# Kernel optimization log

Hardware: AMD Instinct MI355X
Metric: run time of the kernel (lower is better)

Reference implementation:

```python
import jax, jax.numpy as jnp
import numpy as np

D_MODEL = 1024
N_HEADS = 16
HEAD_DIM = D_MODEL // N_HEADS  # 64
ROT = HEAD_DIM // 2            # RotaryEmbedding(dim=head_dim//2) -> rot_dim = 32
THETA = 10000.0
BS, CTX, CACHE_LEN = 8, 1, 4096


def _rope(x, offset):
    """lucidrains rotate_queries_or_keys: rotate first ROT dims of head_dim,
    interleaved pair convention (x0,x1)->(-x1,x0), freqs repeated pairwise."""
    s = x.shape[2]
    inv_freq = 1.0 / (THETA ** (jnp.arange(0, ROT, 2, dtype=jnp.float32) / ROT))  # [ROT//2]
    t = offset + jnp.arange(s, dtype=jnp.float32)
    freqs = jnp.repeat(t[:, None] * inv_freq[None, :], 2, axis=-1)  # [s, ROT]
    cos, sin = jnp.cos(freqs), jnp.sin(freqs)
    x1, x2 = x[..., :ROT], x[..., ROT:]
    xr = x1.reshape(*x1.shape[:-1], ROT // 2, 2)
    rh = jnp.stack([-xr[..., 1], xr[..., 0]], axis=-1).reshape(x1.shape)
    return jnp.concatenate([x1 * cos + rh * sin, x2], axis=-1)


def setup_inputs() -> dict:
    key = jax.random.key(0)
    ks = jax.random.split(key, 11)
    w = lambda k, shp: jax.random.normal(k, shp, dtype=jnp.float32) * 0.02
    return {
        "q": jax.random.normal(ks[0], (BS, CTX, D_MODEL), dtype=jnp.float32),
        "k_cache": jax.random.normal(ks[1], (BS, N_HEADS, CACHE_LEN, HEAD_DIM), dtype=jnp.float32),
        "v_cache": jax.random.normal(ks[2], (BS, N_HEADS, CACHE_LEN, HEAD_DIM), dtype=jnp.float32),
        "WQ_w": w(ks[3], (D_MODEL, D_MODEL)), "WQ_b": w(ks[4], (D_MODEL,)),
        "WK_w": w(ks[5], (D_MODEL, D_MODEL)), "WK_b": w(ks[6], (D_MODEL,)),
        "WV_w": w(ks[7], (D_MODEL, D_MODEL)), "WV_b": w(ks[8], (D_MODEL,)),
        "WO_w": w(ks[9], (D_MODEL, D_MODEL)), "WO_b": w(ks[10], (D_MODEL,)),
    }


def reference(q, k_cache, v_cache, WQ_w, WQ_b, WK_w, WK_b, WV_w, WV_b, WO_w, WO_b):
    bs, context, dim = q.shape
    # last=True path: only the final token queries; k/v computed from the full input
    q_in = q[:, -1:, :]
    offset = (context - 1) + k_cache.shape[2]
    to_heads = lambda x: x.reshape(bs, -1, N_HEADS, HEAD_DIM).transpose(0, 2, 1, 3)
    qh = to_heads(q_in @ WQ_w.T + WQ_b)             # [b,h,1,hd]
    kh = to_heads(q @ WK_w.T + WK_b)                # [b,h,ctx,hd]
    vh = to_heads(q @ WV_w.T + WV_b)
    k = jnp.concatenate([k_cache, kh], axis=2)      # [b,h,S,hd]
    v = jnp.concatenate([v_cache, vh], axis=2)
    q_rot = _rope(qh, offset)
    k_rot = _rope(k, 0)                             # RoPE re-applied to full cache
    scale = 1.0 / np.sqrt(HEAD_DIM)
    scores = jnp.einsum('bhqd,bhkd->bhqk', q_rot, k_rot) * scale
    attn = jax.nn.softmax(scores, axis=-1)          # is_causal=False (decode step)
    out = jnp.einsum('bhqk,bhkd->bhqd', attn, v)
    out = out.transpose(0, 2, 1, 3).reshape(bs, -1, dim)
    return out @ WO_w.T + WO_b
```

## Files before the change

kernel.cpp:

```cpp
#include <hip/hip_runtime.h>
#include <hip/hip_bf16.h>
#include <math.h>

#define NH    16
#define HD    64
#define DM    1024
#define BSZ   8
#define CL    4096
#define SPLIT 8
#define CHUNK (CL / SPLIT)
#define PSTRIDE 68

#define WS_QH   0
#define WS_KH   8192
#define WS_VH   16384
#define WS_QROT 24576
#define WS_KROT 32768
#define WS_PART 40960
#define WS_HEAD (40960 + 128 * SPLIT * PSTRIDE)
#define WS_FLAG (WS_HEAD + 8192)

#define LOG2_THETA 13.287712379549449
#define TWO_PI     6.283185307179586476925286766559
#define SM_SCALE_L2 (0.125f * 1.4426950408889634f)

__device__ __forceinline__ void bf2x(unsigned u, float& a, float& b) {
  union { unsigned i; float f; } lo, hi;
  lo.i = u << 16;
  hi.i = u & 0xffff0000u;
  a = lo.f; b = hi.f;
}

template<int DT> __device__ __forceinline__ void load4(const void* p, long i4, float* o);
template<> __device__ __forceinline__ void load4<0>(const void* p, long i4, float* o) {
  uint2 w = ((const uint2*)p)[i4];
  bf2x(w.x, o[0], o[1]); bf2x(w.y, o[2], o[3]);
}
template<> __device__ __forceinline__ void load4<1>(const void* p, long i4, float* o) {
  float4 f = ((const float4*)p)[i4];
  o[0] = f.x; o[1] = f.y; o[2] = f.z; o[3] = f.w;
}

template<int DT> __device__ __forceinline__ void load8(const void* p, long i8, float* o);
template<> __device__ __forceinline__ void load8<0>(const void* p, long i8, float* o) {
  uint4 u = ((const uint4*)p)[i8];
  bf2x(u.x, o[0], o[1]); bf2x(u.y, o[2], o[3]);
  bf2x(u.z, o[4], o[5]); bf2x(u.w, o[6], o[7]);
}
template<> __device__ __forceinline__ void load8<1>(const void* p, long i8, float* o) {
  const float4* f = (const float4*)p + 2 * i8;
  float4 a = f[0], b = f[1];
  o[0] = a.x; o[1] = a.y; o[2] = a.z; o[3] = a.w;
  o[4] = b.x; o[5] = b.y; o[6] = b.z; o[7] = b.w;
}

template<int DT> __device__ __forceinline__ float ld1(const void* p, int i);
template<> __device__ __forceinline__ float ld1<0>(const void* p, int i) {
  return __bfloat162float(((const __hip_bfloat16*)p)[i]);
}
template<> __device__ __forceinline__ float ld1<1>(const void* p, int i) {
  return ((const float*)p)[i];
}

template<int DT> __device__ __forceinline__ void st1(void* p, int i, float v);
template<> __device__ __forceinline__ void st1<0>(void* p, int i, float v) {
  ((__hip_bfloat16*)p)[i] = __float2bfloat16(v);
}
template<> __device__ __forceinline__ void st1<1>(void* p, int i, float v) {
  ((float*)p)[i] = v;
}

__global__ __launch_bounds__(256) void detect_dtype(const unsigned* __restrict__ qw,
                                                    float* __restrict__ ws)
{
  __shared__ int s;
  if (threadIdx.x == 0) s = 0;
  __syncthreads();
  int bad = 0;
  for (int i = threadIdx.x; i < 4096; i += 256) {
    float a, b;
    bf2x(qw[i], a, b);
    if (!(fabsf(a) < 1e10f) || !(fabsf(b) < 1e10f)) bad = 1;
  }
  if (bad) atomicOr(&s, 1);
  __syncthreads();
  if (threadIdx.x == 0) ((unsigned*)ws)[WS_FLAG] = (unsigned)s;
}

__device__ __forceinline__ bool active(const float* ws, int DT) {
  return ((const unsigned*)ws)[WS_FLAG] == (unsigned)DT;
}

template<int DT>
__global__ __launch_bounds__(256) void qkv_gemv(
    const void* __restrict__ x,
    const void* __restrict__ wq, const void* __restrict__ bq,
    const void* __restrict__ wk, const void* __restrict__ bk,
    const void* __restrict__ wv, const void* __restrict__ bv,
    float* __restrict__ ws)
{
  if (!active(ws, DT)) return;
  const int wid  = threadIdx.x >> 6;
  const int lane = threadIdx.x & 63;
  const int gid  = blockIdx.x * 4 + wid;
  const int proj = gid >> 10;
  const int j    = gid & 1023;

  const void* W  = (proj == 0) ? wq : (proj == 1) ? wk : wv;
  const void* Bb = (proj == 0) ? bq : (proj == 1) ? bk : bv;
  float* dst = ws + ((proj == 0) ? WS_QH : (proj == 1) ? WS_KH : WS_VH);

  float acc[BSZ];
#pragma unroll
  for (int b = 0; b < BSZ; b++) acc[b] = 0.f;

#pragma unroll
  for (int i = 0; i < 4; i++) {
    float wf[4];
    load4<DT>(W, (long)j * 256 + lane + 64 * i, wf);
#pragma unroll
    for (int b = 0; b < BSZ; b++) {
      float xf[4];
      load4<DT>(x, (long)b * 256 + lane + 64 * i, xf);
      acc[b] += wf[0] * xf[0] + wf[1] * xf[1] + wf[2] * xf[2] + wf[3] * xf[3];
    }
  }
#pragma unroll
  for (int b = 0; b < BSZ; b++)
#pragma unroll
    for (int off = 32; off >= 1; off >>= 1)
      acc[b] += __shfl_xor(acc[b], off);

  if (lane == 0) {
    float bias = ld1<DT>(Bb, j);
#pragma unroll
    for (int b = 0; b < BSZ; b++) dst[b * DM + j] = acc[b] + bias;
  }
}

__global__ __launch_bounds__(256) void rope_qk(float* __restrict__ ws)
{
  const int tid    = blockIdx.x * 256 + threadIdx.x;
  const int tensor = tid >> 13;
  const int r      = tid & 8191;
  const int d      = r & 63;

  const float* src = ws + (tensor ? WS_KH : WS_QH);
  float*       dst = ws + (tensor ? WS_KROT : WS_QROT);

  float v = src[r];
  if (d < 32) {
    int j = d >> 1;
    double invf = exp2(-(double)j * (LOG2_THETA / 16.0));
    double ang  = fmod(4096.0 * invf, TWO_PI);
    float c = cosf((float)ang), s = sinf((float)ang);
    float pv = src[r ^ 1];
    v = (d & 1) ? (v * c + pv * s) : (v * c - pv * s);
  }
  dst[r] = v;
}

template<int DT>
__global__ __launch_bounds__(256) void attn_chunks(
    const void* __restrict__ kcache,
    const void* __restrict__ vcache,
    float* __restrict__ ws)
{
  if (!active(ws, DT)) return;
  const int wid  = threadIdx.x >> 6;
  const int lane = threadIdx.x & 63;
  const int bh   = blockIdx.x / SPLIT;
  const int chnk = blockIdx.x % SPLIT;
  const int g    = lane & 7;
  const int pidx = lane >> 3;
  const int t0   = chnk * CHUNK + wid * (CHUNK / 4) + pidx;
  const int NIT  = CHUNK / 4 / 8;

  __shared__ float sm[4], sl[4], so[4][64];

  float qv[8];
  {
    const float* qr = ws + WS_QROT + bh * HD + g * 8;
#pragma unroll
    for (int i = 0; i < 8; i++) qv[i] = qr[i];
  }

  float cc[4], ss[4], c8[4], s8[4];
  {
    const int jb = 4 * (g & 3);
#pragma unroll
    for (int m = 0; m < 4; m++) {
      double invf = exp2(-(double)(jb + m) * (LOG2_THETA / 16.0));
      double a0 = fmod((double)t0 * invf, TWO_PI);
      cc[m] = cosf((float)a0); ss[m] = sinf((float)a0);
      double a8 = fmod(8.0 * invf, TWO_PI);
      c8[m] = cosf((float)a8); s8[m] = sinf((float)a8);
    }
  }

  float m2 = -INFINITY, ll = 0.f;
  float o[8];
#pragma unroll
  for (int i = 0; i < 8; i++) o[i] = 0.f;

  float kcur[8], vcur[8];
  load8<DT>(kcache, ((long)bh * CL + t0) * 8 + g, kcur);
  load8<DT>(vcache, ((long)bh * CL + t0) * 8 + g, vcur);

#pragma unroll
  for (int it = 0; it < 16; it++) {
    const int t = t0 + it * 8;
    float kn[8], vn[8];
#pragma unroll
    for (int i = 0; i < 8; i++) { kn[i] = kcur[i]; vn[i] = vcur[i]; }
    if (it < NIT - 1) {
      load8<DT>(kcache, ((long)bh * CL + t + 8) * 8 + g, kn);
      load8<DT>(vcache, ((long)bh * CL + t + 8) * 8 + g, vn);
    }

    float x[8];
#pragma unroll
    for (int i = 0; i < 8; i++) x[i] = kcur[i];

    if (g < 4) {
#pragma unroll
      for (int m = 0; m < 4; m++) {
        float a = x[2 * m], b = x[2 * m + 1];
        x[2 * m]     = a * cc[m] - b * ss[m];
        x[2 * m + 1] = b * cc[m] + a * ss[m];
        float cn = cc[m] * c8[m] - ss[m] * s8[m];
        float sn = ss[m] * c8[m] + cc[m] * s8[m];
        cc[m] = cn; ss[m] = sn;
      }
    }

    float p = 0.f;
#pragma unroll
    for (int i = 0; i < 8; i++) p += x[i] * qv[i];
    p += __shfl_xor(p, 1);
    p += __shfl_xor(p, 2);
    p += __shfl_xor(p, 4);

    const float s2 = p * SM_SCALE_L2;
    const float mn = fmaxf(m2, s2);
    const float al = exp2f(m2 - mn);
    const float pp = exp2f(s2 - mn);
    ll = ll * al + pp;
#pragma unroll
    for (int i = 0; i < 8; i++) o[i] = o[i] * al + pp * vcur[i];
    m2 = mn;

#pragma unroll
    for (int i = 0; i < 8; i++) { kcur[i] = kn[i]; vcur[i] = vn[i]; }
  }

#pragma unroll
  for (int off = 8; off < 64; off <<= 1) {
    float om  = __shfl_xor(m2, off);
    float olp = __shfl_xor(ll, off);
    float mn  = fmaxf(m2, om);
    float a   = exp2f(m2 - mn);
    float bsc = exp2f(om - mn);
    ll = ll * a + olp * bsc;
#pragma unroll
    for (int i = 0; i < 8; i++) {
      float oo = __shfl_xor(o[i], off);
      o[i] = o[i] * a + oo * bsc;
    }
    m2 = mn;
  }

  if (lane == 0) { sm[wid] = m2; sl[wid] = ll; }
  if (pidx == 0) {
#pragma unroll
    for (int i = 0; i < 8; i++) so[wid][g * 8 + i] = o[i];
  }
  __syncthreads();

  if (wid == 0) {
    float M = fmaxf(fmaxf(sm[0], sm[1]), fmaxf(sm[2], sm[3]));
    float L = 0.f, O = 0.f;
#pragma unroll
    for (int w = 0; w < 4; w++) {
      float sc = exp2f(sm[w] - M);
      L += sc * sl[w];
      O += sc * so[w][lane];
    }
    float* pb = ws + WS_PART + ((size_t)bh * SPLIT + chnk) * PSTRIDE;
    if (lane == 0) { pb[0] = M; pb[1] = L; }
    pb[4 + lane] = O;
  }
}

__global__ __launch_bounds__(256) void combine(float* __restrict__ ws)
{
  const int wid  = threadIdx.x >> 6;
  const int lane = threadIdx.x & 63;
  const int bh   = blockIdx.x * 4 + wid;

  float p = ws[WS_QROT + bh * HD + lane] * ws[WS_KROT + bh * HD + lane];
#pragma unroll
  for (int off = 1; off < 64; off <<= 1) p += __shfl_xor(p, off);
  const float s2 = p * SM_SCALE_L2;

  float M = -INFINITY, L = 0.f, O = 0.f;
  const float* pb = ws + WS_PART + (size_t)bh * SPLIT * PSTRIDE;
#pragma unroll
  for (int pi = 0; pi < SPLIT; pi++) {
    const float* pp = pb + pi * PSTRIDE;
    float mp = pp[0], lp = pp[1], op = pp[4 + lane];
    float mn = fmaxf(M, mp);
    float a  = exp2f(M - mn);
    float bb = exp2f(mp - mn);
    O = O * a + op * bb;
    L = L * a + lp * bb;
    M = mn;
  }
  {
    float vn = ws[WS_VH + bh * HD + lane];
    float mn = fmaxf(M, s2);
    float a  = exp2f(M - mn);
    float pn = exp2f(s2 - mn);
    O = O * a + pn * vn;
    L = L * a + pn;
  }
  ws[WS_HEAD + bh * HD + lane] = O / L;
}

template<int DT>
__global__ __launch_bounds__(256) void out_gemv(
    const float* __restrict__ ws,
    const void* __restrict__ wo,
    const void* __restrict__ bo,
    void* __restrict__ out)
{
  if (!active(ws, DT)) return;
  const int wid  = threadIdx.x >> 6;
  const int lane = threadIdx.x & 63;
  const int j    = blockIdx.x * 4 + wid;

  const float4* Xr = reinterpret_cast<const float4*>(ws + WS_HEAD);

  float acc[BSZ];
#pragma unroll
  for (int b = 0; b < BSZ; b++) acc[b] = 0.f;

#pragma unroll
  for (int i = 0; i < 4; i++) {
    float wf[4];
    load4<DT>(wo, (long)j * 256 + lane + 64 * i, wf);
#pragma unroll
    for (int b = 0; b < BSZ; b++) {
      float4 xf = Xr[b * 256 + lane + 64 * i];
      acc[b] += wf[0] * xf.x + wf[1] * xf.y + wf[2] * xf.z + wf[3] * xf.w;
    }
  }
#pragma unroll
  for (int b = 0; b < BSZ; b++)
#pragma unroll
    for (int off = 32; off >= 1; off >>= 1)
      acc[b] += __shfl_xor(acc[b], off);

  if (lane == 0) {
    float bias = ld1<DT>(bo, j);
#pragma unroll
    for (int b = 0; b < BSZ; b++)
      st1<DT>(out, b * DM + j, acc[b] + bias);
  }
}

extern "C" void kernel_launch(void* const* d_in, const int* in_sizes, int n_in,
                              void* d_out, int out_size, void* d_ws, size_t ws_size,
                              hipStream_t stream)
{
  const void* q  = d_in[0];
  const void* kc = d_in[1];
  const void* vc = d_in[2];
  const void* wq = d_in[3];
  const void* bq = d_in[4];
  const void* wk = d_in[5];
  const void* bk = d_in[6];
  const void* wv = d_in[7];
  const void* bv = d_in[8];
  const void* wo = d_in[9];
  const void* bo = d_in[10];
  float* ws = (float*)d_ws;

  detect_dtype<<<1, 256, 0, stream>>>((const unsigned*)q, ws);

  qkv_gemv<0><<<768, 256, 0, stream>>>(q, wq, bq, wk, bk, wv, bv, ws);
  qkv_gemv<1><<<768, 256, 0, stream>>>(q, wq, bq, wk, bk, wv, bv, ws);

  rope_qk<<<64, 256, 0, stream>>>(ws);

  attn_chunks<0><<<128 * SPLIT, 256, 0, stream>>>(kc, vc, ws);
  attn_chunks<1><<<128 * SPLIT, 256, 0, stream>>>(kc, vc, ws);

  combine<<<32, 256, 0, stream>>>(ws);

  out_gemv<0><<<256, 256, 0, stream>>>(ws, wo, bo, d_out);
  out_gemv<1><<<256, 256, 0, stream>>>(ws, wo, bo, d_out);
}
```

Baseline: 332.2 us.

## Fuse RoPE into attention/combine, drop dtype-detect kernel, two-pass chunk softmax

Removes the separate dtype-detection and rope_qk launches. Each kernel now detects the dtype inline with a wave-level vote, and RoPE on q and on the new k is computed where it is used, in attn_chunks and combine. The attention inner loop is split into two passes: all scores are computed first, then a single max and exp. V is then loaded and accumulated in a second pass with a 4-deep register prefetch ring. This cuts launch overhead and per-step rescaling, at the cost of more registers and reading K and V in separate passes.

```diff
diff --git a/kernel.cpp b/kernel.cpp
--- a/kernel.cpp
+++ b/kernel.cpp
@@ -14,11 +14,8 @@
 #define WS_QH   0
 #define WS_KH   8192
 #define WS_VH   16384
-#define WS_QROT 24576
-#define WS_KROT 32768
 #define WS_PART 40960
 #define WS_HEAD (40960 + 128 * SPLIT * PSTRIDE)
-#define WS_FLAG (WS_HEAD + 8192)
 
 #define LOG2_THETA 13.287712379549449
 #define TWO_PI     6.283185307179586476925286766559
@@ -70,25 +67,10 @@
   ((float*)p)[i] = v;
 }
 
-__global__ __launch_bounds__(256) void detect_dtype(const unsigned* __restrict__ qw,
-                                                    float* __restrict__ ws)
-{
-  __shared__ int s;
-  if (threadIdx.x == 0) s = 0;
-  __syncthreads();
-  int bad = 0;
-  for (int i = threadIdx.x; i < 4096; i += 256) {
-    float a, b;
-    bf2x(qw[i], a, b);
-    if (!(fabsf(a) < 1e10f) || !(fabsf(b) < 1e10f)) bad = 1;
-  }
-  if (bad) atomicOr(&s, 1);
-  __syncthreads();
-  if (threadIdx.x == 0) ((unsigned*)ws)[WS_FLAG] = (unsigned)s;
-}
-
-__device__ __forceinline__ bool active(const float* ws, int DT) {
-  return ((const unsigned*)ws)[WS_FLAG] == (unsigned)DT;
+__device__ __forceinline__ bool data_is_f32(const unsigned* qw) {
+  float a, b;
+  bf2x(qw[threadIdx.x & 63], a, b);
+  return __any(!(fabsf(a) < 1e10f) || !(fabsf(b) < 1e10f)) != 0;
 }
 
 template<int DT>
@@ -99,7 +81,7 @@
     const void* __restrict__ wv, const void* __restrict__ bv,
     float* __restrict__ ws)
 {
-  if (!active(ws, DT)) return;
+  if (data_is_f32((const unsigned*)x) != (DT == 1)) return;
   const int wid  = threadIdx.x >> 6;
   const int lane = threadIdx.x & 63;
   const int gid  = blockIdx.x * 4 + wid;
@@ -138,51 +120,40 @@
   }
 }
 
-__global__ __launch_bounds__(256) void rope_qk(float* __restrict__ ws)
-{
-  const int tid    = blockIdx.x * 256 + threadIdx.x;
-  const int tensor = tid >> 13;
-  const int r      = tid & 8191;
-  const int d      = r & 63;
-
-  const float* src = ws + (tensor ? WS_KH : WS_QH);
-  float*       dst = ws + (tensor ? WS_KROT : WS_QROT);
-
-  float v = src[r];
-  if (d < 32) {
-    int j = d >> 1;
-    double invf = exp2(-(double)j * (LOG2_THETA / 16.0));
-    double ang  = fmod(4096.0 * invf, TWO_PI);
-    float c = cosf((float)ang), s = sinf((float)ang);
-    float pv = src[r ^ 1];
-    v = (d & 1) ? (v * c + pv * s) : (v * c - pv * s);
-  }
-  dst[r] = v;
-}
-
 template<int DT>
 __global__ __launch_bounds__(256) void attn_chunks(
+    const unsigned* __restrict__ qdet,
     const void* __restrict__ kcache,
     const void* __restrict__ vcache,
     float* __restrict__ ws)
 {
-  if (!active(ws, DT)) return;
+  if (data_is_f32(qdet) != (DT == 1)) return;
   const int wid  = threadIdx.x >> 6;
   const int lane = threadIdx.x & 63;
   const int bh   = blockIdx.x / SPLIT;
   const int chnk = blockIdx.x % SPLIT;
   const int g    = lane & 7;
   const int pidx = lane >> 3;
-  const int t0   = chnk * CHUNK + wid * (CHUNK / 4) + pidx;
-  const int NIT  = CHUNK / 4 / 8;
-
-  __shared__ float sm[4], sl[4], so[4][64];
+  const int t0   = chnk * CHUNK + wid * 128 + pidx;
+
+  __shared__ float smx[4], sl[4], so[4][64];
 
   float qv[8];
   {
-    const float* qr = ws + WS_QROT + bh * HD + g * 8;
+    const float* qr = ws + WS_QH + bh * HD + g * 8;
 #pragma unroll
     for (int i = 0; i < 8; i++) qv[i] = qr[i];
+    if (g < 4) {
+#pragma unroll
+      for (int m = 0; m < 4; m++) {
+        double invf = exp2(-(double)(4 * g + m) * (LOG2_THETA / 16.0));
+        double ang  = fmod(4096.0 * invf, TWO_PI);
+        float c = cosf((float)ang), s = sinf((float)ang);
+        float e = qv[2 * m], o = qv[2 * m + 1];
+        qv[2 * m]     = e * c - o * s;
+        qv[2 * m + 1] = o * c + e * s;
+      }
+    }
   }
 
   float cc[4], ss[4], c8[4], s8[4];
@@ -198,29 +169,19 @@
     }
   }
 
-  float m2 = -INFINITY, ll = 0.f;
-  float o[8];
-#pragma unroll
-  for (int i = 0; i < 8; i++) o[i] = 0.f;
-
-  float kcur[8], vcur[8];
-  load8<DT>(kcache, ((long)bh * CL + t0) * 8 + g, kcur);
-  load8<DT>(vcache, ((long)bh * CL + t0) * 8 + g, vcur);
-
-#pragma unroll
-  for (int it = 0; it < 16; it++) {
-    const int t = t0 + it * 8;
-    float kn[8], vn[8];
-#pragma unroll
-    for (int i = 0; i < 8; i++) { kn[i] = kcur[i]; vn[i] = vcur[i]; }
-    if (it < NIT - 1) {
-      load8<DT>(kcache, ((long)bh * CL + t + 8) * 8 + g, kn);
-      load8<DT>(vcache, ((long)bh * CL + t + 8) * 8 + g, vn);
-    }
-
+  const long rbase = (long)bh * CL + t0;
+
+  float kr[4][8];
+#pragma unroll
+  for (int i = 0; i < 4; i++) load8<DT>(kcache, (rbase + 8 * i) * 8 + g, kr[i]);
+
+  float s[16];
+#pragma unroll
+  for (int o = 0; o < 16; o++) {
     float x[8];
 #pragma unroll
-    for (int i = 0; i < 8; i++) x[i] = kcur[i];
+    for (int i = 0; i < 8; i++) x[i] = kr[o & 3][i];
+    if (o + 4 < 16) load8<DT>(kcache, (rbase + 8 * (o + 4)) * 8 + g, kr[o & 3]);
 
     if (g < 4) {
 #pragma unroll
@@ -240,18 +201,31 @@
     p += __shfl_xor(p, 1);
     p += __shfl_xor(p, 2);
     p += __shfl_xor(p, 4);
-
-    const float s2 = p * SM_SCALE_L2;
-    const float mn = fmaxf(m2, s2);
-    const float al = exp2f(m2 - mn);
-    const float pp = exp2f(s2 - mn);
-    ll = ll * al + pp;
-#pragma unroll
-    for (int i = 0; i < 8; i++) o[i] = o[i] * al + pp * vcur[i];
-    m2 = mn;
-
-#pragma unroll
-    for (int i = 0; i < 8; i++) { kcur[i] = kn[i]; vcur[i] = vn[i]; }
+    s[o] = p * SM_SCALE_L2;
+  }
+
+  float m2 = s[0];
+#pragma unroll
+  for (int o = 1; o < 16; o++) m2 = fmaxf(m2, s[o]);
+  float ll = 0.f;
+#pragma unroll
+  for (int o = 0; o < 16; o++) { s[o] = exp2f(s[o] - m2); ll += s[o]; }
+
+  float vr[4][8];
+#pragma unroll
+  for (int i = 0; i < 4; i++) load8<DT>(vcache, (rbase + 8 * i) * 8 + g, vr[i]);
+
+  float oa[8];
+#pragma unroll
+  for (int i = 0; i < 8; i++) oa[i] = 0.f;
+#pragma unroll
+  for (int o = 0; o < 16; o++) {
+    float v[8];
+#pragma unroll
+    for (int i = 0; i < 8; i++) v[i] = vr[o & 3][i];
+    if (o + 4 < 16) load8<DT>(vcache, (rbase + 8 * (o + 4)) * 8 + g, vr[o & 3]);
+#pragma unroll
+    for (int i = 0; i < 8; i++) oa[i] = fmaf(s[o], v[i], oa[i]);
   }
 
 #pragma unroll
@@ -264,25 +238,25 @@
     ll = ll * a + olp * bsc;
 #pragma unroll
     for (int i = 0; i < 8; i++) {
-      float oo = __shfl_xor(o[i], off);
-      o[i] = o[i] * a + oo * bsc;
+      float oo = __shfl_xor(oa[i], off);
+      oa[i] = oa[i] * a + oo * bsc;
     }
     m2 = mn;
   }
 
-  if (lane == 0) { sm[wid] = m2; sl[wid] = ll; }
+  if (lane == 0) { smx[wid] = m2; sl[wid] = ll; }
   if (pidx == 0) {
 #pragma unroll
-    for (int i = 0; i < 8; i++) so[wid][g * 8 + i] = o[i];
+    for (int i = 0; i < 8; i++) so[wid][g * 8 + i] = oa[i];
   }
   __syncthreads();
 
   if (wid == 0) {
-    float M = fmaxf(fmaxf(sm[0], sm[1]), fmaxf(sm[2], sm[3]));
+    float M = fmaxf(fmaxf(smx[0], smx[1]), fmaxf(smx[2], smx[3]));
     float L = 0.f, O = 0.f;
 #pragma unroll
     for (int w = 0; w < 4; w++) {
-      float sc = exp2f(sm[w] - M);
+      float sc = exp2f(smx[w] - M);
       L += sc * sl[w];
       O += sc * so[w][lane];
     }
@@ -298,7 +272,21 @@
   const int lane = threadIdx.x & 63;
   const int bh   = blockIdx.x * 4 + wid;
 
-  float p = ws[WS_QROT + bh * HD + lane] * ws[WS_KROT + bh * HD + lane];
+  float qd = ws[WS_QH + bh * HD + lane];
+  float kd = ws[WS_KH + bh * HD + lane];
+  float qp = ws[WS_QH + bh * HD + (lane ^ 1)];
+  float kp = ws[WS_KH + bh * HD + (lane ^ 1)];
+  float qrot = qd, krot = kd;
+  if (lane < 32) {
+    int j = lane >> 1;
+    double invf = exp2(-(double)j * (LOG2_THETA / 16.0));
+    double ang  = fmod(4096.0 * invf, TWO_PI);
+    float c = cosf((float)ang), s = sinf((float)ang);
+    if (lane & 1) { qrot = qd * c + qp * s; krot = kd * c + kp * s; }
+    else          { qrot = qd * c - qp * s; krot = kd * c - kp * s; }
+  }
+
+  float p = qrot * krot;
 #pragma unroll
   for (int off = 1; off < 64; off <<= 1) p += __shfl_xor(p, off);
   const float s2 = p * SM_SCALE_L2;
@@ -329,12 +317,13 @@
 
 template<int DT>
 __global__ __launch_bounds__(256) void out_gemv(
+    const unsigned* __restrict__ qdet,
     const float* __restrict__ ws,
     const void* __restrict__ wo,
     const void* __restrict__ bo,
     void* __restrict__ out)
 {
-  if (!active(ws, DT)) return;
+  if (data_is_f32(qdet) != (DT == 1)) return;
   const int wid  = threadIdx.x >> 6;
   const int lane = threadIdx.x & 63;
   const int j    = blockIdx.x * 4 + wid;
@@ -385,19 +374,16 @@
   const void* wo = d_in[9];
   const void* bo = d_in[10];
   float* ws = (float*)d_ws;
-
-  detect_dtype<<<1, 256, 0, stream>>>((const unsigned*)q, ws);
+  const unsigned* qdet = (const unsigned*)q;
 
   qkv_gemv<0><<<768, 256, 0, stream>>>(q, wq, bq, wk, bk, wv, bv, ws);
   qkv_gemv<1><<<768, 256, 0, stream>>>(q, wq, bq, wk, bk, wv, bv, ws);
 
-  rope_qk<<<64, 256, 0, stream>>>(ws);
-
-  attn_chunks<0><<<128 * SPLIT, 256, 0, stream>>>(kc, vc, ws);
-  attn_chunks<1><<<128 * SPLIT, 256, 0, stream>>>(kc, vc, ws);
+  attn_chunks<0><<<128 * SPLIT, 256, 0, stream>>>(qdet, kc, vc, ws);
+  attn_chunks<1><<<128 * SPLIT, 256, 0, stream>>>(qdet, kc, vc, ws);
 
   combine<<<32, 256, 0, stream>>>(ws);
 
-  out_gemv<0><<<256, 256, 0, stream>>>(ws, wo, bo, d_out);
-  out_gemv<1><<<256, 256, 0, stream>>>(ws, wo, bo, d_out);
-}
+  out_gemv<0><<<256, 256, 0, stream>>>(qdet, ws, wo, bo, d_out);
+  out_gemv<1><<<256, 256, 0, stream>>>(qdet, ws, wo, bo, d_out);
+}
```

Result: faster. 322.8 us (-2.9%).
